# Performance work log

Measured on AMD Instinct MI355X. Metric: run time of the kernel, lower is better.

The kernel has to match this reference:

```python
import jax, jax.numpy as jnp
import numpy as np

TOP_K = 2


def setup_inputs() -> dict:
    key = jax.random.key(0)
    ks = jax.random.split(key, 5)
    B, S, D, F, E = 4, 2048, 1024, 2048, 8
    sd = 1.0 / np.sqrt(D)
    sf = 1.0 / np.sqrt(F)
    return {
        "hidden_states": jax.random.normal(ks[0], (B, S, D), jnp.float32),
        "router_w1": jax.random.normal(ks[1], (D, 128), jnp.float32) * sd,
        "router_w2": jax.random.normal(ks[2], (128, E), jnp.float32) * (1.0 / np.sqrt(128)),
        "W1": jax.random.normal(ks[3], (E, D, F), jnp.float32) * sd,
        "W2": jax.random.normal(ks[4], (E, F, D), jnp.float32) * sf,
    }


def reference(hidden_states, router_w1, router_w2, W1, W2):
    B, S, D = hidden_states.shape
    E = W1.shape[0]
    # --- Router: MLP -> softmax -> top-k -> renormalize ---
    router_logits = jax.nn.silu(hidden_states @ router_w1) @ router_w2  # (B,S,E)
    router_probs = jax.nn.softmax(router_logits, axis=-1)
    top_vals, top_idx = jax.lax.top_k(router_probs, TOP_K)  # (B,S,K)
    routing_weights = top_vals / jnp.sum(top_vals, axis=-1, keepdims=True)

    # --- Dispatch/combine as dense combine-weight matrix (faithful to
    # weighted scatter-add combine in _grouped_expert_forward) ---
    T = B * S
    x = hidden_states.reshape(T, D)
    idx = top_idx.reshape(T, TOP_K)
    w = routing_weights.reshape(T, TOP_K).astype(hidden_states.dtype)
    combine = jnp.zeros((T, E), hidden_states.dtype).at[
        jnp.arange(T)[:, None], idx
    ].add(w)  # (T,E)

    # --- Per-expert FFN on all tokens, then weighted combine ---
    h = jax.nn.silu(jnp.einsum("td,edf->tef", x, W1))  # (T,E,F)
    expert_out = jnp.einsum("tef,efd->ted", h, W2)      # (T,E,D)
    out = jnp.einsum("te,ted->td", combine, expert_out)
    return out.reshape(B, S, D)
```

## Files before the change

kernel.cpp:

```cpp
#include <hip/hip_runtime.h>
#include <hip/hip_bf16.h>
#include <math.h>

#define T_TOK 8192
#define E_NUM 8
#define GAP_TAU 2e-3f

typedef __attribute__((ext_vector_type(8))) short short8;
typedef __attribute__((ext_vector_type(4))) float floatx4;

__device__ __forceinline__ unsigned short f2bf(float f) {
  unsigned int u = __builtin_bit_cast(unsigned int, f);
  u += 0x7fffu + ((u >> 16) & 1u);
  return (unsigned short)(u >> 16);
}

__device__ __forceinline__ void async16(const unsigned short* g, unsigned short* l) {
  __builtin_amdgcn_global_load_lds(
      (const __attribute__((address_space(1))) void*)g,
      (__attribute__((address_space(3))) void*)l, 16, 0, 0);
}

__device__ __forceinline__ bool tile_map(int flat, const int* cnt, int nt_log2,
                                         int& e, int& m0, int& n0) {
  const int xcd = flat & 7;
  const int idx = flat >> 3;
  int mtp[E_NUM + 1];
  mtp[0] = 0;
#pragma unroll
  for (int q = 0; q < E_NUM; ++q) mtp[q + 1] = mtp[q] + ((cnt[q] + 127) >> 7);
  const int MT = mtp[E_NUM];
  const int band = (MT + 7) >> 3;
  const int i = idx >> nt_log2;
  if (i >= band) return false;
  const int g = xcd * band + i;
  if (g >= MT) return false;
  e = 0;
#pragma unroll
  for (int q = 0; q < E_NUM - 1; ++q) if (g >= mtp[q + 1]) e = q + 1;
  m0 = (g - mtp[e]) << 7;
  n0 = (idx & ((1 << nt_log2) - 1)) << 7;
  return true;
}

__global__ __launch_bounds__(256) void router_fp32_kernel(
    const float* __restrict__ x, const float* __restrict__ rw1,
    const float* __restrict__ rw2,
    int* __restrict__ tok_top, float* __restrict__ tok_w,
    int* __restrict__ fix_list, int* __restrict__ fix_cnt,
    unsigned short* __restrict__ xb) {
  __shared__ __align__(16) float xs[8][1024];
  __shared__ float ph[128][8];
  __shared__ float hs[8][129];
  __shared__ float ls[8][8];
  const int t = threadIdx.x;
  const int tok0 = blockIdx.x * 8;

  {
    const float4* xsrc = (const float4*)(x + (size_t)tok0 * 1024);
    float4* xd = (float4*)&xs[0][0];
    ushort4* xbd = (ushort4*)(xb + (size_t)tok0 * 1024);
#pragma unroll
    for (int i = 0; i < 8; ++i) {
      float4 v = xsrc[t + i * 256];
      xd[t + i * 256] = v;
      ushort4 o;
      o.x = f2bf(v.x); o.y = f2bf(v.y); o.z = f2bf(v.z); o.w = f2bf(v.w);
      xbd[t + i * 256] = o;
    }
  }
  __syncthreads();

  const int j = t & 127, h = t >> 7;
  float acc[8];
#pragma unroll
  for (int tt = 0; tt < 8; ++tt) acc[tt] = 0.f;

  const int dbeg = h * 512, dend = dbeg + 512;
#pragma unroll 2
  for (int d0 = dbeg; d0 < dend; d0 += 4) {
    float w0 = rw1[(d0 + 0) * 128 + j];
    float w1 = rw1[(d0 + 1) * 128 + j];
    float w2 = rw1[(d0 + 2) * 128 + j];
    float w3 = rw1[(d0 + 3) * 128 + j];
    float4 xv[8];
#pragma unroll
    for (int tt = 0; tt < 8; ++tt) xv[tt] = *(const float4*)&xs[tt][d0];
#pragma unroll
    for (int tt = 0; tt < 8; ++tt) {
      acc[tt] = fmaf(xv[tt].x, w0, acc[tt]);
      acc[tt] = fmaf(xv[tt].y, w1, acc[tt]);
      acc[tt] = fmaf(xv[tt].z, w2, acc[tt]);
      acc[tt] = fmaf(xv[tt].w, w3, acc[tt]);
    }
  }
  if (h == 1) {
#pragma unroll
    for (int tt = 0; tt < 8; ++tt) ph[j][tt] = acc[tt];
  }
  __syncthreads();
  if (h == 0) {
#pragma unroll
    for (int tt = 0; tt < 8; ++tt) {
      float a = acc[tt] + ph[j][tt];
      hs[tt][j] = a / (1.f + expf(-a));
    }
  }
  __syncthreads();
  if (t < 64) {
    int tt = t >> 3, e = t & 7;
    float l = 0.f;
#pragma unroll 4
    for (int jj = 0; jj < 128; ++jj) l = fmaf(hs[tt][jj], rw2[jj * 8 + e], l);
    ls[tt][e] = l;
  }
  __syncthreads();
  if (t < 8) {
    int tt = t;
    float l[8];
#pragma unroll
    for (int e = 0; e < 8; ++e) l[e] = ls[tt][e];
    int i0 = 0;
#pragma unroll
    for (int e = 1; e < 8; ++e) if (l[e] > l[i0]) i0 = e;
    int i1 = (i0 == 0) ? 1 : 0;
#pragma unroll
    for (int e = 0; e < 8; ++e) if (e != i0 && l[e] > l[i1]) i1 = e;
    float v2 = -3.4e38f;
#pragma unroll
    for (int e = 0; e < 8; ++e) if (e != i0 && e != i1 && l[e] > v2) v2 = l[e];
    float gap = l[i1] - v2;
    float p = expf(l[i1] - l[i0]);
    float w0 = 1.f / (1.f + p);
    int tok = tok0 + tt;
    tok_top[2 * tok] = i0; tok_top[2 * tok + 1] = i1;
    tok_w[2 * tok] = w0;   tok_w[2 * tok + 1] = 1.f - w0;
    if (gap < GAP_TAU) { int pos = atomicAdd(fix_cnt, 1); fix_list[pos] = tok; }
  }
}

__global__ __launch_bounds__(256) void router_fix_kernel(
    const float* __restrict__ x, const float* __restrict__ rw1,
    const float* __restrict__ rw2, const int* __restrict__ fix_list,
    const int* __restrict__ fix_cnt,
    int* __restrict__ tok_top, float* __restrict__ tok_w) {
  __shared__ __align__(16) float xs[1024];
  __shared__ double red[128];
  __shared__ double hs[128];
  __shared__ double ls[8];
  const int t = threadIdx.x;
  const int nfix = *fix_cnt;
  for (int it = blockIdx.x; it < nfix; it += gridDim.x) {
    int tok = fix_list[it];
    ((float4*)xs)[t] = ((const float4*)(x + (size_t)tok * 1024))[t];
    __syncthreads();
    const int j = t & 127, h = t >> 7;
    double a0 = 0, a1 = 0, a2 = 0, a3 = 0;
    const int dbeg = h * 512;
    for (int d0 = dbeg; d0 < dbeg + 512; d0 += 4) {
      a0 = fma((double)xs[d0 + 0], (double)rw1[(d0 + 0) * 128 + j], a0);
      a1 = fma((double)xs[d0 + 1], (double)rw1[(d0 + 1) * 128 + j], a1);
      a2 = fma((double)xs[d0 + 2], (double)rw1[(d0 + 2) * 128 + j], a2);
      a3 = fma((double)xs[d0 + 3], (double)rw1[(d0 + 3) * 128 + j], a3);
    }
    double a = (a0 + a1) + (a2 + a3);
    if (h == 1) red[j] = a;
    __syncthreads();
    if (h == 0) {
      double s = a + red[j];
      hs[j] = s / (1.0 + exp(-s));
    }
    __syncthreads();
    if (t < 8) {
      int e = t;
      double l = 0;
      for (int jj = 0; jj < 128; ++jj) l = fma(hs[jj], (double)rw2[jj * 8 + e], l);
      ls[e] = l;
    }
    __syncthreads();
    if (t == 0) {
      double l[8];
#pragma unroll
      for (int e = 0; e < 8; ++e) l[e] = ls[e];
      int i0 = 0;
#pragma unroll
      for (int e = 1; e < 8; ++e) if (l[e] > l[i0]) i0 = e;
      int i1 = (i0 == 0) ? 1 : 0;
#pragma unroll
      for (int e = 0; e < 8; ++e) if (e != i0 && l[e] > l[i1]) i1 = e;
      double p = exp(l[i1] - l[i0]);
      double w0 = 1.0 / (1.0 + p);
      tok_top[2 * tok] = i0; tok_top[2 * tok + 1] = i1;
      tok_w[2 * tok] = (float)w0; tok_w[2 * tok + 1] = (float)(1.0 - w0);
    }
    __syncthreads();
  }
}

__global__ __launch_bounds__(256) void scatter_kernel(
    const int* __restrict__ tok_top, const float* __restrict__ tok_w,
    int* __restrict__ cnt, int* __restrict__ tid_list, float* __restrict__ tw_list) {
  __shared__ int hist[8], run[8];
  const int t = threadIdx.x;
  if (t < 8) hist[t] = 0;
  __syncthreads();
  const int tok = blockIdx.x * 256 + t;
  const int e0 = tok_top[2 * tok], e1 = tok_top[2 * tok + 1];
  atomicAdd(&hist[e0], 1);
  atomicAdd(&hist[e1], 1);
  __syncthreads();
  if (t < 8) run[t] = atomicAdd(&cnt[t], hist[t]);
  __syncthreads();
  int p0 = atomicAdd(&run[e0], 1);
  tid_list[e0 * T_TOK + p0] = tok; tw_list[e0 * T_TOK + p0] = tok_w[2 * tok];
  int p1 = atomicAdd(&run[e1], 1);
  tid_list[e1 * T_TOK + p1] = tok; tw_list[e1 * T_TOK + p1] = tok_w[2 * tok + 1];
}

__global__ void prefix_kernel(const int* __restrict__ cnt, int* __restrict__ base) {
  if (threadIdx.x == 0 && blockIdx.x == 0) {
    int s = 0;
    for (int e = 0; e < E_NUM; ++e) { base[e] = s; s += cnt[e]; }
  }
}

__global__ __launch_bounds__(256) void transpose_bf16_kernel(
    const float* __restrict__ in, unsigned short* __restrict__ out, int R, int C) {
  __shared__ unsigned short tile[64][65];
  const int e = blockIdx.z;
  const int r0 = blockIdx.y * 64, c0 = blockIdx.x * 64;
  const float* src = in + (size_t)e * R * C;
  unsigned short* dst = out + (size_t)e * R * C;
  const int t = threadIdx.x;
  const int cc = (t & 15) * 4;
#pragma unroll
  for (int p = 0; p < 4; ++p) {
    int r = p * 16 + (t >> 4);
    float4 v = *(const float4*)(src + (size_t)(r0 + r) * C + c0 + cc);
    tile[cc + 0][r] = f2bf(v.x);
    tile[cc + 1][r] = f2bf(v.y);
    tile[cc + 2][r] = f2bf(v.z);
    tile[cc + 3][r] = f2bf(v.w);
  }
  __syncthreads();
#pragma unroll
  for (int p = 0; p < 4; ++p) {
    int fr = p * 16 + (t >> 4);
    ushort4 o;
    o.x = tile[fr][cc + 0]; o.y = tile[fr][cc + 1];
    o.z = tile[fr][cc + 2]; o.w = tile[fr][cc + 3];
    *(ushort4*)(dst + (size_t)(c0 + fr) * R + r0 + cc) = o;
  }
}

__global__ __launch_bounds__(256) void gemm1_kernel(
    const unsigned short* __restrict__ xb,
    const unsigned short* __restrict__ w1t,
    const int* __restrict__ cnt, const int* __restrict__ base,
    const int* __restrict__ tid_list,
    unsigned short* __restrict__ h_buf) {
  int e, m0, n0;
  if (!tile_map(blockIdx.x, cnt, 4, e, m0, n0)) return;
  const int count = cnt[e];
  const int bs = base[e];

  __shared__ __align__(16) unsigned short As[128 * 64];
  __shared__ __align__(16) unsigned short Bs[128 * 64];

  const int t = threadIdx.x;
  const int wv = t >> 6, lane = t & 63;
  const int quad = lane >> 4, lr = lane & 15;
  const int wm = (wv & 1) * 64, wn = (wv >> 1) * 64;
  const int lr8 = lane >> 3, lc8 = lane & 7;
  const int chunk = lc8 ^ lr8;

  const unsigned short* aptr[4];
  const unsigned short* bptr[4];
#pragma unroll
  for (int q = 0; q < 4; ++q) {
    int ar = m0 + wv * 32 + q * 8 + lr8;
    int ai = ar < count ? ar : count - 1;
    int tok = tid_list[e * T_TOK + ai];
    aptr[q] = xb + (size_t)tok * 1024 + chunk * 8;
    int br = n0 + wv * 32 + q * 8 + lr8;
    bptr[q] = w1t + ((size_t)e * 2048 + br) * 1024 + chunk * 8;
  }
  unsigned short* aldsb = &As[wv * 2048];
  unsigned short* bldsb = &Bs[wv * 2048];

  floatx4 zero = {0.f, 0.f, 0.f, 0.f};
  floatx4 acc[4][4];
#pragma unroll
  for (int i = 0; i < 4; ++i)
#pragma unroll
    for (int j = 0; j < 4; ++j) acc[i][j] = zero;

  for (int k0 = 0; k0 < 1024; k0 += 64) {
    __syncthreads();
#pragma unroll
    for (int q = 0; q < 4; ++q) {
      async16(aptr[q] + k0, aldsb + q * 512);
      async16(bptr[q] + k0, bldsb + q * 512);
    }
    __syncthreads();
#pragma unroll
    for (int ks = 0; ks < 2; ++ks) {
      short8 af[4], bfv[4];
#pragma unroll
      for (int i = 0; i < 4; ++i) {
        int r = wm + i * 16 + lr;
        int pc = (ks * 4 + quad) ^ (lr & 7);
        af[i] = *(const short8*)&As[r * 64 + pc * 8];
      }
#pragma unroll
      for (int j = 0; j < 4; ++j) {
        int r = wn + j * 16 + lr;
        int pc = (ks * 4 + quad) ^ (lr & 7);
        bfv[j] = *(const short8*)&Bs[r * 64 + pc * 8];
      }
#pragma unroll
      for (int i = 0; i < 4; ++i)
#pragma unroll
        for (int j = 0; j < 4; ++j)
          acc[i][j] = __builtin_amdgcn_mfma_f32_16x16x32_bf16(af[i], bfv[j], acc[i][j], 0, 0, 0);
    }
  }

#pragma unroll
  for (int i = 0; i < 4; ++i) {
#pragma unroll
    for (int r = 0; r < 4; ++r) {
      int grow = m0 + wm + i * 16 + quad * 4 + r;
      if (grow < count) {
        size_t rowoff = (size_t)(bs + grow) * 2048;
#pragma unroll
        for (int j = 0; j < 4; ++j) {
          float v = acc[i][j][r];
          float s = v / (1.0f + __expf(-v));
          h_buf[rowoff + n0 + wn + j * 16 + lr] = f2bf(s);
        }
      }
    }
  }
}

__global__ __launch_bounds__(256) void gemm2_kernel(
    const unsigned short* __restrict__ h_buf,
    const unsigned short* __restrict__ w2t,
    const int* __restrict__ cnt, const int* __restrict__ base,
    const int* __restrict__ tid_list, const float* __restrict__ tw_list,
    float* __restrict__ out) {
  int e, m0, n0;
  if (!tile_map(blockIdx.x, cnt, 3, e, m0, n0)) return;
  const int count = cnt[e];
  const int bs = base[e];

  __shared__ __align__(16) unsigned short As[128 * 64];
  __shared__ __align__(16) unsigned short Bs[128 * 64];

  const int t = threadIdx.x;
  const int wv = t >> 6, lane = t & 63;
  const int quad = lane >> 4, lr = lane & 15;
  const int wm = (wv & 1) * 64, wn = (wv >> 1) * 64;
  const int lr8 = lane >> 3, lc8 = lane & 7;
  const int chunk = lc8 ^ lr8;

  const unsigned short* aptr[4];
  const unsigned short* bptr[4];
#pragma unroll
  for (int q = 0; q < 4; ++q) {
    int ar = m0 + wv * 32 + q * 8 + lr8;
    int ai = ar < count ? ar : count - 1;
    aptr[q] = h_buf + (size_t)(bs + ai) * 2048 + chunk * 8;
    int br = n0 + wv * 32 + q * 8 + lr8;
    bptr[q] = w2t + ((size_t)e * 1024 + br) * 2048 + chunk * 8;
  }
  unsigned short* aldsb = &As[wv * 2048];
  unsigned short* bldsb = &Bs[wv * 2048];

  floatx4 zero = {0.f, 0.f, 0.f, 0.f};
  floatx4 acc[4][4];
#pragma unroll
  for (int i = 0; i < 4; ++i)
#pragma unroll
    for (int j = 0; j < 4; ++j) acc[i][j] = zero;

  for (int k0 = 0; k0 < 2048; k0 += 64) {
    __syncthreads();
#pragma unroll
    for (int q = 0; q < 4; ++q) {
      async16(aptr[q] + k0, aldsb + q * 512);
      async16(bptr[q] + k0, bldsb + q * 512);
    }
    __syncthreads();
#pragma unroll
    for (int ks = 0; ks < 2; ++ks) {
      short8 af[4], bfv[4];
#pragma unroll
      for (int i = 0; i < 4; ++i) {
        int r = wm + i * 16 + lr;
        int pc = (ks * 4 + quad) ^ (lr & 7);
        af[i] = *(const short8*)&As[r * 64 + pc * 8];
      }
#pragma unroll
      for (int j = 0; j < 4; ++j) {
        int r = wn + j * 16 + lr;
        int pc = (ks * 4 + quad) ^ (lr & 7);
        bfv[j] = *(const short8*)&Bs[r * 64 + pc * 8];
      }
#pragma unroll
      for (int i = 0; i < 4; ++i)
#pragma unroll
        for (int j = 0; j < 4; ++j)
          acc[i][j] = __builtin_amdgcn_mfma_f32_16x16x32_bf16(af[i], bfv[j], acc[i][j], 0, 0, 0);
    }
  }

#pragma unroll
  for (int i = 0; i < 4; ++i) {
#pragma unroll
    for (int r = 0; r < 4; ++r) {
      int grow = m0 + wm + i * 16 + quad * 4 + r;
      if (grow < count) {
        int tok = tid_list[e * T_TOK + grow];
        float w = tw_list[e * T_TOK + grow];
        size_t rowoff = (size_t)tok * 1024;
#pragma unroll
        for (int j = 0; j < 4; ++j) {
          unsafeAtomicAdd(&out[rowoff + n0 + wn + j * 16 + lr], acc[i][j][r] * w);
        }
      }
    }
  }
}

extern "C" void kernel_launch(void* const* d_in, const int* in_sizes, int n_in,
                              void* d_out, int out_size, void* d_ws, size_t ws_size,
                              hipStream_t stream) {
  const float* x   = (const float*)d_in[0];
  const float* rw1 = (const float*)d_in[1];
  const float* rw2 = (const float*)d_in[2];
  const float* W1  = (const float*)d_in[3];
  const float* W2  = (const float*)d_in[4];
  float* out = (float*)d_out;

  char* ws = (char*)d_ws;
  int*            cnt      = (int*)(ws + 0);
  int*            base     = (int*)(ws + 64);
  int*            fix_cnt  = (int*)(ws + 128);
  int*            tid_list = (int*)(ws + 512);
  float*          tw_list  = (float*)(ws + 262656);
  unsigned short* xb       = (unsigned short*)(ws + 524800);
  unsigned short* w1t      = (unsigned short*)(ws + 17302016);
  unsigned short* w2t      = (unsigned short*)(ws + 50856448);
  unsigned short* hbuf     = (unsigned short*)(ws + 84410880);
  int*            tok_top  = (int*)(ws + 151519744);
  float*          tok_w    = (float*)(ws + 151585280);
  int*            fix_list = (int*)(ws + 151650816);

  hipMemsetAsync(d_out, 0, (size_t)T_TOK * 1024 * 4, stream);
  hipMemsetAsync(ws, 0, 192, stream);

  hipLaunchKernelGGL(router_fp32_kernel, dim3(1024), dim3(256), 0, stream,
                     x, rw1, rw2, tok_top, tok_w, fix_list, fix_cnt, xb);
  hipLaunchKernelGGL(router_fix_kernel, dim3(128), dim3(256), 0, stream,
                     x, rw1, rw2, fix_list, fix_cnt, tok_top, tok_w);
  hipLaunchKernelGGL(scatter_kernel, dim3(32), dim3(256), 0, stream,
                     tok_top, tok_w, cnt, tid_list, tw_list);
  hipLaunchKernelGGL(prefix_kernel, dim3(1), dim3(1), 0, stream, cnt, base);
  hipLaunchKernelGGL(transpose_bf16_kernel, dim3(32, 16, 8), dim3(256), 0, stream,
                     W1, w1t, 1024, 2048);
  hipLaunchKernelGGL(transpose_bf16_kernel, dim3(16, 32, 8), dim3(256), 0, stream,
                     W2, w2t, 2048, 1024);
  hipLaunchKernelGGL(gemm1_kernel, dim3(2176), dim3(256), 0, stream,
                     xb, w1t, cnt, base, tid_list, hbuf);
  hipLaunchKernelGGL(gemm2_kernel, dim3(1088), dim3(256), 0, stream,
                     hbuf, w2t, cnt, base, tid_list, tw_list, out);
}
```

Before: 556.2 us.

## Use 256x256 tiles with 512 threads and double-buffered LDS in expert GEMMs

Both grouped expert GEMMs move from 128x128 tiles with 256 threads to 256x256 tiles with 8 waves, each wave computing 128x64. The K-loop now double-buffers LDS, issuing the async loads for the next K slice before computing the current one, which removes one barrier per iteration. The XCD-aware tile mapping is replaced by a plain m/n block decomposition. Larger tiles raise operand reuse and cut global traffic, but they use 128KB of LDS and 128 accumulator registers per thread, which lowers occupancy. The grid also shrinks to 576 and 288 blocks, which risks uneven load across CUs.

```diff
diff --git a/kernel.cpp b/kernel.cpp
--- a/kernel.cpp
+++ b/kernel.cpp
@@ -19,28 +19,6 @@
   __builtin_amdgcn_global_load_lds(
       (const __attribute__((address_space(1))) void*)g,
       (__attribute__((address_space(3))) void*)l, 16, 0, 0);
-}
-
-__device__ __forceinline__ bool tile_map(int flat, const int* cnt, int nt_log2,
-                                         int& e, int& m0, int& n0) {
-  const int xcd = flat & 7;
-  const int idx = flat >> 3;
-  int mtp[E_NUM + 1];
-  mtp[0] = 0;
-#pragma unroll
-  for (int q = 0; q < E_NUM; ++q) mtp[q + 1] = mtp[q] + ((cnt[q] + 127) >> 7);
-  const int MT = mtp[E_NUM];
-  const int band = (MT + 7) >> 3;
-  const int i = idx >> nt_log2;
-  if (i >= band) return false;
-  const int g = xcd * band + i;
-  if (g >= MT) return false;
-  e = 0;
-#pragma unroll
-  for (int q = 0; q < E_NUM - 1; ++q) if (g >= mtp[q + 1]) e = q + 1;
-  m0 = (g - mtp[e]) << 7;
-  n0 = (idx & ((1 << nt_log2) - 1)) << 7;
-  return true;
 }
 
 __global__ __launch_bounds__(256) void router_fp32_kernel(
@@ -253,24 +231,34 @@
   }
 }
 
-__global__ __launch_bounds__(256) void gemm1_kernel(
+__global__ __launch_bounds__(512) void gemm1_kernel(
     const unsigned short* __restrict__ xb,
     const unsigned short* __restrict__ w1t,
     const int* __restrict__ cnt, const int* __restrict__ base,
     const int* __restrict__ tid_list,
     unsigned short* __restrict__ h_buf) {
-  int e, m0, n0;
-  if (!tile_map(blockIdx.x, cnt, 4, e, m0, n0)) return;
+  __shared__ __align__(16) unsigned short lds[4][256 * 64];
+
+  int mtp[E_NUM + 1];
+  mtp[0] = 0;
+#pragma unroll
+  for (int q = 0; q < E_NUM; ++q) mtp[q + 1] = mtp[q] + ((cnt[q] + 255) >> 8);
+  const int MT = mtp[E_NUM];
+  const int n = blockIdx.x & 7;
+  const int m = blockIdx.x >> 3;
+  if (m >= MT) return;
+  int e = 0;
+#pragma unroll
+  for (int q = 0; q < E_NUM - 1; ++q) if (m >= mtp[q + 1]) e = q + 1;
+  const int m0 = (m - mtp[e]) << 8;
+  const int n0 = n << 8;
   const int count = cnt[e];
   const int bs = base[e];
-
-  __shared__ __align__(16) unsigned short As[128 * 64];
-  __shared__ __align__(16) unsigned short Bs[128 * 64];
 
   const int t = threadIdx.x;
   const int wv = t >> 6, lane = t & 63;
   const int quad = lane >> 4, lr = lane & 15;
-  const int wm = (wv & 1) * 64, wn = (wv >> 1) * 64;
+  const int wr = (wv & 1) * 128, wc = (wv >> 1) * 64;
   const int lr8 = lane >> 3, lc8 = lane & 7;
   const int chunk = lc8 ^ lr8;
 
@@ -285,83 +273,107 @@
     int br = n0 + wv * 32 + q * 8 + lr8;
     bptr[q] = w1t + ((size_t)e * 2048 + br) * 1024 + chunk * 8;
   }
-  unsigned short* aldsb = &As[wv * 2048];
-  unsigned short* bldsb = &Bs[wv * 2048];
+  const int ldsoff = wv * 2048;
 
   floatx4 zero = {0.f, 0.f, 0.f, 0.f};
-  floatx4 acc[4][4];
-#pragma unroll
-  for (int i = 0; i < 4; ++i)
+  floatx4 acc[8][4];
+#pragma unroll
+  for (int i = 0; i < 8; ++i)
 #pragma unroll
     for (int j = 0; j < 4; ++j) acc[i][j] = zero;
 
-  for (int k0 = 0; k0 < 1024; k0 += 64) {
-    __syncthreads();
-#pragma unroll
-    for (int q = 0; q < 4; ++q) {
-      async16(aptr[q] + k0, aldsb + q * 512);
-      async16(bptr[q] + k0, bldsb + q * 512);
-    }
-    __syncthreads();
-#pragma unroll
-    for (int ks = 0; ks < 2; ++ks) {
-      short8 af[4], bfv[4];
-#pragma unroll
-      for (int i = 0; i < 4; ++i) {
-        int r = wm + i * 16 + lr;
-        int pc = (ks * 4 + quad) ^ (lr & 7);
-        af[i] = *(const short8*)&As[r * 64 + pc * 8];
-      }
-#pragma unroll
-      for (int j = 0; j < 4; ++j) {
-        int r = wn + j * 16 + lr;
-        int pc = (ks * 4 + quad) ^ (lr & 7);
-        bfv[j] = *(const short8*)&Bs[r * 64 + pc * 8];
-      }
-#pragma unroll
-      for (int i = 0; i < 4; ++i)
-#pragma unroll
-        for (int j = 0; j < 4; ++j)
-          acc[i][j] = __builtin_amdgcn_mfma_f32_16x16x32_bf16(af[i], bfv[j], acc[i][j], 0, 0, 0);
-    }
-  }
-
-#pragma unroll
-  for (int i = 0; i < 4; ++i) {
+  unsigned short *Ac = lds[0], *Bc = lds[1], *An = lds[2], *Bn = lds[3];
+
+#define G1_STAGE(Ab, Bb, K0)                                \
+  do {                                                      \
+    _Pragma("unroll")                                       \
+    for (int q = 0; q < 4; ++q) {                           \
+      async16(aptr[q] + (K0), (Ab) + ldsoff + q * 512);     \
+      async16(bptr[q] + (K0), (Bb) + ldsoff + q * 512);     \
+    }                                                       \
+  } while (0)
+
+#define G1_COMPUTE(Ab, Bb)                                                    \
+  do {                                                                        \
+    _Pragma("unroll")                                                         \
+    for (int ks = 0; ks < 2; ++ks) {                                          \
+      short8 af[8], bfv[4];                                                   \
+      int pc = (ks * 4 + quad) ^ (lr & 7);                                    \
+      _Pragma("unroll")                                                       \
+      for (int i = 0; i < 8; ++i)                                             \
+        af[i] = *(const short8*)&(Ab)[(wr + i * 16 + lr) * 64 + pc * 8];      \
+      _Pragma("unroll")                                                       \
+      for (int j = 0; j < 4; ++j)                                             \
+        bfv[j] = *(const short8*)&(Bb)[(wc + j * 16 + lr) * 64 + pc * 8];     \
+      _Pragma("unroll")                                                       \
+      for (int i = 0; i < 8; ++i)                                             \
+        _Pragma("unroll")                                                     \
+        for (int j = 0; j < 4; ++j)                                           \
+          acc[i][j] = __builtin_amdgcn_mfma_f32_16x16x32_bf16(af[i], bfv[j],  \
+                                                              acc[i][j], 0, 0, 0); \
+    }                                                                         \
+  } while (0)
+
+  G1_STAGE(Ac, Bc, 0);
+  __syncthreads();
+  for (int k0 = 64; k0 < 1024; k0 += 64) {
+    G1_STAGE(An, Bn, k0);
+    G1_COMPUTE(Ac, Bc);
+    __syncthreads();
+    unsigned short* tmp;
+    tmp = Ac; Ac = An; An = tmp;
+    tmp = Bc; Bc = Bn; Bn = tmp;
+  }
+  G1_COMPUTE(Ac, Bc);
+
+#pragma unroll
+  for (int i = 0; i < 8; ++i) {
 #pragma unroll
     for (int r = 0; r < 4; ++r) {
-      int grow = m0 + wm + i * 16 + quad * 4 + r;
+      int grow = m0 + wr + i * 16 + quad * 4 + r;
       if (grow < count) {
         size_t rowoff = (size_t)(bs + grow) * 2048;
 #pragma unroll
         for (int j = 0; j < 4; ++j) {
           float v = acc[i][j][r];
           float s = v / (1.0f + __expf(-v));
-          h_buf[rowoff + n0 + wn + j * 16 + lr] = f2bf(s);
+          h_buf[rowoff + n0 + wc + j * 16 + lr] = f2bf(s);
         }
       }
     }
   }
-}
-
-__global__ __launch_bounds__(256) void gemm2_kernel(
+#undef G1_STAGE
+#undef G1_COMPUTE
+}
+
+__global__ __launch_bounds__(512) void gemm2_kernel(
     const unsigned short* __restrict__ h_buf,
     const unsigned short* __restrict__ w2t,
     const int* __restrict__ cnt, const int* __restrict__ base,
     const int* __restrict__ tid_list, const float* __restrict__ tw_list,
     float* __restrict__ out) {
-  int e, m0, n0;
-  if (!tile_map(blockIdx.x, cnt, 3, e, m0, n0)) return;
+  __shared__ __align__(16) unsigned short lds[4][256 * 64];
+
+  int mtp[E_NUM + 1];
+  mtp[0] = 0;
+#pragma unroll
+  for (int q = 0; q < E_NUM; ++q) mtp[q + 1] = mtp[q] + ((cnt[q] + 255) >> 8);
+  const int MT = mtp[E_NUM];
+  const int n = blockIdx.x & 3;
+  const int m = blockIdx.x >> 2;
+  if (m >= MT) return;
+  int e = 0;
+#pragma unroll
+  for (int q = 0; q < E_NUM - 1; ++q) if (m >= mtp[q + 1]) e = q + 1;
+  const int m0 = (m - mtp[e]) << 8;
+  const int n0 = n << 8;
   const int count = cnt[e];
   const int bs = base[e];
-
-  __shared__ __align__(16) unsigned short As[128 * 64];
-  __shared__ __align__(16) unsigned short Bs[128 * 64];
 
   const int t = threadIdx.x;
   const int wv = t >> 6, lane = t & 63;
   const int quad = lane >> 4, lr = lane & 15;
-  const int wm = (wv & 1) * 64, wn = (wv >> 1) * 64;
+  const int wr = (wv & 1) * 128, wc = (wv >> 1) * 64;
   const int lr8 = lane >> 3, lc8 = lane & 7;
   const int chunk = lc8 ^ lr8;
 
@@ -375,63 +387,77 @@
     int br = n0 + wv * 32 + q * 8 + lr8;
     bptr[q] = w2t + ((size_t)e * 1024 + br) * 2048 + chunk * 8;
   }
-  unsigned short* aldsb = &As[wv * 2048];
-  unsigned short* bldsb = &Bs[wv * 2048];
+  const int ldsoff = wv * 2048;
 
   floatx4 zero = {0.f, 0.f, 0.f, 0.f};
-  floatx4 acc[4][4];
-#pragma unroll
-  for (int i = 0; i < 4; ++i)
+  floatx4 acc[8][4];
+#pragma unroll
+  for (int i = 0; i < 8; ++i)
 #pragma unroll
     for (int j = 0; j < 4; ++j) acc[i][j] = zero;
 
-  for (int k0 = 0; k0 < 2048; k0 += 64) {
-    __syncthreads();
-#pragma unroll
-    for (int q = 0; q < 4; ++q) {
-      async16(aptr[q] + k0, aldsb + q * 512);
-      async16(bptr[q] + k0, bldsb + q * 512);
-    }
-    __syncthreads();
-#pragma unroll
-    for (int ks = 0; ks < 2; ++ks) {
-      short8 af[4], bfv[4];
-#pragma unroll
-      for (int i = 0; i < 4; ++i) {
-        int r = wm + i * 16 + lr;
-        int pc = (ks * 4 + quad) ^ (lr & 7);
-        af[i] = *(const short8*)&As[r * 64 + pc * 8];
-      }
-#pragma unroll
-      for (int j = 0; j < 4; ++j) {
-        int r = wn + j * 16 + lr;
-        int pc = (ks * 4 + quad) ^ (lr & 7);
-        bfv[j] = *(const short8*)&Bs[r * 64 + pc * 8];
-      }
-#pragma unroll
-      for (int i = 0; i < 4; ++i)
-#pragma unroll
-        for (int j = 0; j < 4; ++j)
-          acc[i][j] = __builtin_amdgcn_mfma_f32_16x16x32_bf16(af[i], bfv[j], acc[i][j], 0, 0, 0);
-    }
-  }
-
-#pragma unroll
-  for (int i = 0; i < 4; ++i) {
+  unsigned short *Ac = lds[0], *Bc = lds[1], *An = lds[2], *Bn = lds[3];
+
+#define G2_STAGE(Ab, Bb, K0)                                \
+  do {                                                      \
+    _Pragma("unroll")                                       \
+    for (int q = 0; q < 4; ++q) {                           \
+      async16(aptr[q] + (K0), (Ab) + ldsoff + q * 512);     \
+      async16(bptr[q] + (K0), (Bb) + ldsoff + q * 512);     \
+    }                                                       \
+  } while (0)
+
+#define G2_COMPUTE(Ab, Bb)                                                    \
+  do {                                                                        \
+    _Pragma("unroll")                                                         \
+    for (int ks = 0; ks < 2; ++ks) {                                          \
+      short8 af[8], bfv[4];                                                   \
+      int pc = (ks * 4 + quad) ^ (lr & 7);                                    \
+      _Pragma("unroll")                                                       \
+      for (int i = 0; i < 8; ++i)                                             \
+        af[i] = *(const short8*)&(Ab)[(wr + i * 16 + lr) * 64 + pc * 8];      \
+      _Pragma("unroll")                                                       \
+      for (int j = 0; j < 4; ++j)                                             \
+        bfv[j] = *(const short8*)&(Bb)[(wc + j * 16 + lr) * 64 + pc * 8];     \
+      _Pragma("unroll")                                                       \
+      for (int i = 0; i < 8; ++i)                                             \
+        _Pragma("unroll")                                                     \
+        for (int j = 0; j < 4; ++j)                                           \
+          acc[i][j] = __builtin_amdgcn_mfma_f32_16x16x32_bf16(af[i], bfv[j],  \
+                                                              acc[i][j], 0, 0, 0); \
+    }                                                                         \
+  } while (0)
+
+  G2_STAGE(Ac, Bc, 0);
+  __syncthreads();
+  for (int k0 = 64; k0 < 2048; k0 += 64) {
+    G2_STAGE(An, Bn, k0);
+    G2_COMPUTE(Ac, Bc);
+    __syncthreads();
+    unsigned short* tmp;
+    tmp = Ac; Ac = An; An = tmp;
+    tmp = Bc; Bc = Bn; Bn = tmp;
+  }
+  G2_COMPUTE(Ac, Bc);
+
+#pragma unroll
+  for (int i = 0; i < 8; ++i) {
 #pragma unroll
     for (int r = 0; r < 4; ++r) {
-      int grow = m0 + wm + i * 16 + quad * 4 + r;
+      int grow = m0 + wr + i * 16 + quad * 4 + r;
       if (grow < count) {
         int tok = tid_list[e * T_TOK + grow];
         float w = tw_list[e * T_TOK + grow];
         size_t rowoff = (size_t)tok * 1024;
 #pragma unroll
         for (int j = 0; j < 4; ++j) {
-          unsafeAtomicAdd(&out[rowoff + n0 + wn + j * 16 + lr], acc[i][j][r] * w);
+          unsafeAtomicAdd(&out[rowoff + n0 + wc + j * 16 + lr], acc[i][j][r] * w);
         }
       }
     }
   }
+#undef G2_STAGE
+#undef G2_COMPUTE
 }
 
 extern "C" void kernel_launch(void* const* d_in, const int* in_sizes, int n_in,
@@ -472,8 +498,8 @@
                      W1, w1t, 1024, 2048);
   hipLaunchKernelGGL(transpose_bf16_kernel, dim3(16, 32, 8), dim3(256), 0, stream,
                      W2, w2t, 2048, 1024);
-  hipLaunchKernelGGL(gemm1_kernel, dim3(2176), dim3(256), 0, stream,
+  hipLaunchKernelGGL(gemm1_kernel, dim3(576), dim3(512), 0, stream,
                      xb, w1t, cnt, base, tid_list, hbuf);
-  hipLaunchKernelGGL(gemm2_kernel, dim3(1088), dim3(256), 0, stream,
+  hipLaunchKernelGGL(gemm2_kernel, dim3(288), dim3(512), 0, stream,
                      hbuf, w2t, cnt, base, tid_list, tw_list, out);
 }
```

New measurement: 559.4 us. About the same (+0.6%).

## Pin each expert to one XCD with persistent tile loops in expert GEMMs

Applied to the files above, without the earlier changes.

Replaces the flat banded tile map with a scheme where blockIdx&7 selects the expert, so every block for an expert lands on the same XCD. Each block then loops persistently over that expert's M×N tiles with a fixed stride, which keeps the expert's weights in that XCD's L2. The transpose kernels move to a 1D grid with the expert in the low bits for the same XCD affinity, and the bf16 copy of x is written with nontemporal stores. The trade-off is that an uneven token split across experts can leave some XCDs doing much more work than others.

```diff
diff --git a/kernel.cpp b/kernel.cpp
--- a/kernel.cpp
+++ b/kernel.cpp
@@ -8,6 +8,7 @@
 
 typedef __attribute__((ext_vector_type(8))) short short8;
 typedef __attribute__((ext_vector_type(4))) float floatx4;
+typedef __attribute__((ext_vector_type(2))) unsigned int uintx2;
 
 __device__ __forceinline__ unsigned short f2bf(float f) {
   unsigned int u = __builtin_bit_cast(unsigned int, f);
@@ -19,28 +20,6 @@
   __builtin_amdgcn_global_load_lds(
       (const __attribute__((address_space(1))) void*)g,
       (__attribute__((address_space(3))) void*)l, 16, 0, 0);
-}
-
-__device__ __forceinline__ bool tile_map(int flat, const int* cnt, int nt_log2,
-                                         int& e, int& m0, int& n0) {
-  const int xcd = flat & 7;
-  const int idx = flat >> 3;
-  int mtp[E_NUM + 1];
-  mtp[0] = 0;
-#pragma unroll
-  for (int q = 0; q < E_NUM; ++q) mtp[q + 1] = mtp[q] + ((cnt[q] + 127) >> 7);
-  const int MT = mtp[E_NUM];
-  const int band = (MT + 7) >> 3;
-  const int i = idx >> nt_log2;
-  if (i >= band) return false;
-  const int g = xcd * band + i;
-  if (g >= MT) return false;
-  e = 0;
-#pragma unroll
-  for (int q = 0; q < E_NUM - 1; ++q) if (g >= mtp[q + 1]) e = q + 1;
-  m0 = (g - mtp[e]) << 7;
-  n0 = (idx & ((1 << nt_log2) - 1)) << 7;
-  return true;
 }
 
 __global__ __launch_bounds__(256) void router_fp32_kernel(
@@ -59,14 +38,14 @@
   {
     const float4* xsrc = (const float4*)(x + (size_t)tok0 * 1024);
     float4* xd = (float4*)&xs[0][0];
-    ushort4* xbd = (ushort4*)(xb + (size_t)tok0 * 1024);
+    uintx2* xbd = (uintx2*)(xb + (size_t)tok0 * 1024);
 #pragma unroll
     for (int i = 0; i < 8; ++i) {
       float4 v = xsrc[t + i * 256];
       xd[t + i * 256] = v;
       ushort4 o;
       o.x = f2bf(v.x); o.y = f2bf(v.y); o.z = f2bf(v.z); o.w = f2bf(v.w);
-      xbd[t + i * 256] = o;
+      __builtin_nontemporal_store(__builtin_bit_cast(uintx2, o), &xbd[t + i * 256]);
     }
   }
   __syncthreads();
@@ -225,10 +204,14 @@
 }
 
 __global__ __launch_bounds__(256) void transpose_bf16_kernel(
-    const float* __restrict__ in, unsigned short* __restrict__ out, int R, int C) {
+    const float* __restrict__ in, unsigned short* __restrict__ out,
+    int R, int C, int ylog) {
   __shared__ unsigned short tile[64][65];
-  const int e = blockIdx.z;
-  const int r0 = blockIdx.y * 64, c0 = blockIdx.x * 64;
+  const int b = blockIdx.x;
+  const int e = b & 7;
+  const int t2 = b >> 3;
+  const int r0 = (t2 & ((1 << ylog) - 1)) << 6;
+  const int c0 = (t2 >> ylog) << 6;
   const float* src = in + (size_t)e * R * C;
   unsigned short* dst = out + (size_t)e * R * C;
   const int t = threadIdx.x;
@@ -259,13 +242,13 @@
     const int* __restrict__ cnt, const int* __restrict__ base,
     const int* __restrict__ tid_list,
     unsigned short* __restrict__ h_buf) {
-  int e, m0, n0;
-  if (!tile_map(blockIdx.x, cnt, 4, e, m0, n0)) return;
-  const int count = cnt[e];
-  const int bs = base[e];
-
   __shared__ __align__(16) unsigned short As[128 * 64];
   __shared__ __align__(16) unsigned short Bs[128 * 64];
+
+  const int e = blockIdx.x & 7;
+  const int count = cnt[e];
+  const int mt = (count + 127) >> 7;
+  const int bs = base[e];
 
   const int t = threadIdx.x;
   const int wv = t >> 6, lane = t & 63;
@@ -274,70 +257,79 @@
   const int lr8 = lane >> 3, lc8 = lane & 7;
   const int chunk = lc8 ^ lr8;
 
-  const unsigned short* aptr[4];
-  const unsigned short* bptr[4];
-#pragma unroll
-  for (int q = 0; q < 4; ++q) {
-    int ar = m0 + wv * 32 + q * 8 + lr8;
-    int ai = ar < count ? ar : count - 1;
-    int tok = tid_list[e * T_TOK + ai];
-    aptr[q] = xb + (size_t)tok * 1024 + chunk * 8;
-    int br = n0 + wv * 32 + q * 8 + lr8;
-    bptr[q] = w1t + ((size_t)e * 2048 + br) * 1024 + chunk * 8;
-  }
-  unsigned short* aldsb = &As[wv * 2048];
-  unsigned short* bldsb = &Bs[wv * 2048];
-
-  floatx4 zero = {0.f, 0.f, 0.f, 0.f};
-  floatx4 acc[4][4];
-#pragma unroll
-  for (int i = 0; i < 4; ++i)
-#pragma unroll
-    for (int j = 0; j < 4; ++j) acc[i][j] = zero;
-
-  for (int k0 = 0; k0 < 1024; k0 += 64) {
-    __syncthreads();
+  for (int idx = blockIdx.x >> 3; idx < mt * 16; idx += 352) {
+    const int nl = idx & 7;
+    int mr = idx >> 3;
+    int nh = 0;
+    if (mr >= mt) { mr -= mt; nh = 1; }
+    const int m0 = mr << 7;
+    const int n0 = (nh * 8 + nl) << 7;
+
+    const unsigned short* aptr[4];
+    const unsigned short* bptr[4];
 #pragma unroll
     for (int q = 0; q < 4; ++q) {
-      async16(aptr[q] + k0, aldsb + q * 512);
-      async16(bptr[q] + k0, bldsb + q * 512);
-    }
-    __syncthreads();
-#pragma unroll
-    for (int ks = 0; ks < 2; ++ks) {
-      short8 af[4], bfv[4];
-#pragma unroll
-      for (int i = 0; i < 4; ++i) {
-        int r = wm + i * 16 + lr;
-        int pc = (ks * 4 + quad) ^ (lr & 7);
-        af[i] = *(const short8*)&As[r * 64 + pc * 8];
-      }
-#pragma unroll
-      for (int j = 0; j < 4; ++j) {
-        int r = wn + j * 16 + lr;
-        int pc = (ks * 4 + quad) ^ (lr & 7);
-        bfv[j] = *(const short8*)&Bs[r * 64 + pc * 8];
-      }
-#pragma unroll
-      for (int i = 0; i < 4; ++i)
-#pragma unroll
-        for (int j = 0; j < 4; ++j)
-          acc[i][j] = __builtin_amdgcn_mfma_f32_16x16x32_bf16(af[i], bfv[j], acc[i][j], 0, 0, 0);
-    }
-  }
-
-#pragma unroll
-  for (int i = 0; i < 4; ++i) {
-#pragma unroll
-    for (int r = 0; r < 4; ++r) {
-      int grow = m0 + wm + i * 16 + quad * 4 + r;
-      if (grow < count) {
-        size_t rowoff = (size_t)(bs + grow) * 2048;
+      int ar = m0 + wv * 32 + q * 8 + lr8;
+      int ai = ar < count ? ar : count - 1;
+      int tok = tid_list[e * T_TOK + ai];
+      aptr[q] = xb + (size_t)tok * 1024 + chunk * 8;
+      int br = n0 + wv * 32 + q * 8 + lr8;
+      bptr[q] = w1t + ((size_t)e * 2048 + br) * 1024 + chunk * 8;
+    }
+    unsigned short* aldsb = &As[wv * 2048];
+    unsigned short* bldsb = &Bs[wv * 2048];
+
+    floatx4 zero = {0.f, 0.f, 0.f, 0.f};
+    floatx4 acc[4][4];
+#pragma unroll
+    for (int i = 0; i < 4; ++i)
+#pragma unroll
+      for (int j = 0; j < 4; ++j) acc[i][j] = zero;
+
+    for (int k0 = 0; k0 < 1024; k0 += 64) {
+      __syncthreads();
+#pragma unroll
+      for (int q = 0; q < 4; ++q) {
+        async16(aptr[q] + k0, aldsb + q * 512);
+        async16(bptr[q] + k0, bldsb + q * 512);
+      }
+      __syncthreads();
+#pragma unroll
+      for (int ks = 0; ks < 2; ++ks) {
+        short8 af[4], bfv[4];
+#pragma unroll
+        for (int i = 0; i < 4; ++i) {
+          int r = wm + i * 16 + lr;
+          int pc = (ks * 4 + quad) ^ (lr & 7);
+          af[i] = *(const short8*)&As[r * 64 + pc * 8];
+        }
 #pragma unroll
         for (int j = 0; j < 4; ++j) {
-          float v = acc[i][j][r];
-          float s = v / (1.0f + __expf(-v));
-          h_buf[rowoff + n0 + wn + j * 16 + lr] = f2bf(s);
+          int r = wn + j * 16 + lr;
+          int pc = (ks * 4 + quad) ^ (lr & 7);
+          bfv[j] = *(const short8*)&Bs[r * 64 + pc * 8];
+        }
+#pragma unroll
+        for (int i = 0; i < 4; ++i)
+#pragma unroll
+          for (int j = 0; j < 4; ++j)
+            acc[i][j] = __builtin_amdgcn_mfma_f32_16x16x32_bf16(af[i], bfv[j], acc[i][j], 0, 0, 0);
+      }
+    }
+
+#pragma unroll
+    for (int i = 0; i < 4; ++i) {
+#pragma unroll
+      for (int r = 0; r < 4; ++r) {
+        int grow = m0 + wm + i * 16 + quad * 4 + r;
+        if (grow < count) {
+          size_t rowoff = (size_t)(bs + grow) * 2048;
+#pragma unroll
+          for (int j = 0; j < 4; ++j) {
+            float v = acc[i][j][r];
+            float s = v / (1.0f + __expf(-v));
+            h_buf[rowoff + n0 + wn + j * 16 + lr] = f2bf(s);
+          }
         }
       }
     }
@@ -350,13 +342,13 @@
     const int* __restrict__ cnt, const int* __restrict__ base,
     const int* __restrict__ tid_list, const float* __restrict__ tw_list,
     float* __restrict__ out) {
-  int e, m0, n0;
-  if (!tile_map(blockIdx.x, cnt, 3, e, m0, n0)) return;
-  const int count = cnt[e];
-  const int bs = base[e];
-
   __shared__ __align__(16) unsigned short As[128 * 64];
   __shared__ __align__(16) unsigned short Bs[128 * 64];
+
+  const int e = blockIdx.x & 7;
+  const int count = cnt[e];
+  const int mt = (count + 127) >> 7;
+  const int bs = base[e];
 
   const int t = threadIdx.x;
   const int wv = t >> 6, lane = t & 63;
@@ -365,69 +357,78 @@
   const int lr8 = lane >> 3, lc8 = lane & 7;
   const int chunk = lc8 ^ lr8;
 
-  const unsigned short* aptr[4];
-  const unsigned short* bptr[4];
-#pragma unroll
-  for (int q = 0; q < 4; ++q) {
-    int ar = m0 + wv * 32 + q * 8 + lr8;
-    int ai = ar < count ? ar : count - 1;
-    aptr[q] = h_buf + (size_t)(bs + ai) * 2048 + chunk * 8;
-    int br = n0 + wv * 32 + q * 8 + lr8;
-    bptr[q] = w2t + ((size_t)e * 1024 + br) * 2048 + chunk * 8;
-  }
-  unsigned short* aldsb = &As[wv * 2048];
-  unsigned short* bldsb = &Bs[wv * 2048];
-
-  floatx4 zero = {0.f, 0.f, 0.f, 0.f};
-  floatx4 acc[4][4];
-#pragma unroll
-  for (int i = 0; i < 4; ++i)
-#pragma unroll
-    for (int j = 0; j < 4; ++j) acc[i][j] = zero;
-
-  for (int k0 = 0; k0 < 2048; k0 += 64) {
-    __syncthreads();
+  for (int idx = blockIdx.x >> 3; idx < mt * 8; idx += 176) {
+    const int nl = idx & 3;
+    int mr = idx >> 2;
+    int nh = 0;
+    if (mr >= mt) { mr -= mt; nh = 1; }
+    const int m0 = mr << 7;
+    const int n0 = (nh * 4 + nl) << 7;
+
+    const unsigned short* aptr[4];
+    const unsigned short* bptr[4];
 #pragma unroll
     for (int q = 0; q < 4; ++q) {
-      async16(aptr[q] + k0, aldsb + q * 512);
-      async16(bptr[q] + k0, bldsb + q * 512);
-    }
-    __syncthreads();
-#pragma unroll
-    for (int ks = 0; ks < 2; ++ks) {
-      short8 af[4], bfv[4];
-#pragma unroll
-      for (int i = 0; i < 4; ++i) {
-        int r = wm + i * 16 + lr;
-        int pc = (ks * 4 + quad) ^ (lr & 7);
-        af[i] = *(const short8*)&As[r * 64 + pc * 8];
-      }
-#pragma unroll
-      for (int j = 0; j < 4; ++j) {
-        int r = wn + j * 16 + lr;
-        int pc = (ks * 4 + quad) ^ (lr & 7);
-        bfv[j] = *(const short8*)&Bs[r * 64 + pc * 8];
-      }
-#pragma unroll
-      for (int i = 0; i < 4; ++i)
-#pragma unroll
-        for (int j = 0; j < 4; ++j)
-          acc[i][j] = __builtin_amdgcn_mfma_f32_16x16x32_bf16(af[i], bfv[j], acc[i][j], 0, 0, 0);
-    }
-  }
-
-#pragma unroll
-  for (int i = 0; i < 4; ++i) {
-#pragma unroll
-    for (int r = 0; r < 4; ++r) {
-      int grow = m0 + wm + i * 16 + quad * 4 + r;
-      if (grow < count) {
-        int tok = tid_list[e * T_TOK + grow];
-        float w = tw_list[e * T_TOK + grow];
-        size_t rowoff = (size_t)tok * 1024;
+      int ar = m0 + wv * 32 + q * 8 + lr8;
+      int ai = ar < count ? ar : count - 1;
+      aptr[q] = h_buf + (size_t)(bs + ai) * 2048 + chunk * 8;
+      int br = n0 + wv * 32 + q * 8 + lr8;
+      bptr[q] = w2t + ((size_t)e * 1024 + br) * 2048 + chunk * 8;
+    }
+    unsigned short* aldsb = &As[wv * 2048];
+    unsigned short* bldsb = &Bs[wv * 2048];
+
+    floatx4 zero = {0.f, 0.f, 0.f, 0.f};
+    floatx4 acc[4][4];
+#pragma unroll
+    for (int i = 0; i < 4; ++i)
+#pragma unroll
+      for (int j = 0; j < 4; ++j) acc[i][j] = zero;
+
+    for (int k0 = 0; k0 < 2048; k0 += 64) {
+      __syncthreads();
+#pragma unroll
+      for (int q = 0; q < 4; ++q) {
+        async16(aptr[q] + k0, aldsb + q * 512);
+        async16(bptr[q] + k0, bldsb + q * 512);
+      }
+      __syncthreads();
+#pragma unroll
+      for (int ks = 0; ks < 2; ++ks) {
+        short8 af[4], bfv[4];
+#pragma unroll
+        for (int i = 0; i < 4; ++i) {
+          int r = wm + i * 16 + lr;
+          int pc = (ks * 4 + quad) ^ (lr & 7);
+          af[i] = *(const short8*)&As[r * 64 + pc * 8];
+        }
 #pragma unroll
         for (int j = 0; j < 4; ++j) {
-          unsafeAtomicAdd(&out[rowoff + n0 + wn + j * 16 + lr], acc[i][j][r] * w);
+          int r = wn + j * 16 + lr;
+          int pc = (ks * 4 + quad) ^ (lr & 7);
+          bfv[j] = *(const short8*)&Bs[r * 64 + pc * 8];
+        }
+#pragma unroll
+        for (int i = 0; i < 4; ++i)
+#pragma unroll
+          for (int j = 0; j < 4; ++j)
+            acc[i][j] = __builtin_amdgcn_mfma_f32_16x16x32_bf16(af[i], bfv[j], acc[i][j], 0, 0, 0);
+      }
+    }
+
+#pragma unroll
+    for (int i = 0; i < 4; ++i) {
+#pragma unroll
+      for (int r = 0; r < 4; ++r) {
+        int grow = m0 + wm + i * 16 + quad * 4 + r;
+        if (grow < count) {
+          int tok = tid_list[e * T_TOK + grow];
+          float w = tw_list[e * T_TOK + grow];
+          size_t rowoff = (size_t)tok * 1024;
+#pragma unroll
+          for (int j = 0; j < 4; ++j) {
+            unsafeAtomicAdd(&out[rowoff + n0 + wn + j * 16 + lr], acc[i][j][r] * w);
+          }
         }
       }
     }
@@ -468,12 +469,12 @@
   hipLaunchKernelGGL(scatter_kernel, dim3(32), dim3(256), 0, stream,
                      tok_top, tok_w, cnt, tid_list, tw_list);
   hipLaunchKernelGGL(prefix_kernel, dim3(1), dim3(1), 0, stream, cnt, base);
-  hipLaunchKernelGGL(transpose_bf16_kernel, dim3(32, 16, 8), dim3(256), 0, stream,
-                     W1, w1t, 1024, 2048);
-  hipLaunchKernelGGL(transpose_bf16_kernel, dim3(16, 32, 8), dim3(256), 0, stream,
-                     W2, w2t, 2048, 1024);
-  hipLaunchKernelGGL(gemm1_kernel, dim3(2176), dim3(256), 0, stream,
+  hipLaunchKernelGGL(transpose_bf16_kernel, dim3(4096), dim3(256), 0, stream,
+                     W1, w1t, 1024, 2048, 4);
+  hipLaunchKernelGGL(transpose_bf16_kernel, dim3(4096), dim3(256), 0, stream,
+                     W2, w2t, 2048, 1024, 5);
+  hipLaunchKernelGGL(gemm1_kernel, dim3(2816), dim3(256), 0, stream,
                      xb, w1t, cnt, base, tid_list, hbuf);
-  hipLaunchKernelGGL(gemm2_kernel, dim3(1088), dim3(256), 0, stream,
+  hipLaunchKernelGGL(gemm2_kernel, dim3(1408), dim3(256), 0, stream,
                      hbuf, w2t, cnt, base, tid_list, tw_list, out);
 }
```

After: 634.5 us. +14.1%, slower.
